# Kernel tuning notes

Hardware: AMD Instinct MI355X
Metric: run time of the kernel (lower is better)

The kernel has to match this reference:

```python
import jax, jax.numpy as jnp
import numpy as np

B, N, H, T = 4096, 512, 1024, 10  # batch, input_size, hidden_size, num_iterations
NUM_OPS = 20


def setup_inputs() -> dict:
    key = jax.random.key(0)
    k1, k2, k3, k4 = jax.random.split(key, 4)
    return {
        "x": jax.random.normal(k1, (B, N, 1), jnp.float32),
        "frozen_weight": jax.random.normal(k2, (1, N, H), jnp.float32) / np.sqrt(H),
        "alpha": jax.random.normal(k3, (T, NUM_OPS), jnp.float32),
        "layer_beta": jax.random.normal(k4, (T, 2), jnp.float32),
    }


def _softshrink(x, lam):
    return jnp.where(x > lam, x - lam, jnp.where(x < -lam, x + lam, jnp.zeros_like(x)))


def _hardshrink(x, lam):
    return jnp.where(jnp.abs(x) > lam, x, jnp.zeros_like(x))


def _make_ops(lam):
    # Same 20 ops, same order as the torch ModuleList.
    return [
        lambda x: _softshrink(x, lam),                 # Softshrink(0.001/L)
        jax.nn.relu,                                   # ReLU
        lambda x: x,                                   # Identity
        lambda x: jax.nn.gelu(x, approximate=False),   # GELU (exact erf, torch default)
        jax.nn.elu,                                    # ELU
        lambda x: _hardshrink(x, lam),                 # Hardshrink(0.001/L)
        lambda x: jnp.clip(x, -1.0, 1.0),              # Hardtanh
        jax.nn.hard_swish,                             # Hardswish
        jax.nn.selu,                                   # SELU
        jax.nn.celu,                                   # CELU
        jax.nn.leaky_relu,                             # LeakyReLU (slope 0.01)
        jax.nn.log_sigmoid,                            # LogSigmoid
        lambda x: x - jnp.tanh(x),                     # Tanhshrink
        jax.nn.soft_sign,                              # Softsign
        jax.nn.softplus,                               # Softplus
        jnp.tanh,                                      # Tanh
        jax.nn.sigmoid,                                # Sigmoid
        jax.nn.hard_sigmoid,                           # Hardsigmoid
        jax.nn.silu,                                   # SiLU
        lambda x: x * jnp.tanh(jax.nn.softplus(x)),    # Mish
    ]


def _forward(x, frozen_weight, alpha, layer_beta):
    W = frozen_weight[0]                       # [N, H]
    L = jnp.linalg.norm(W, ord=2) ** 2         # spectral norm squared (Lipschitz)
    lam = 0.001 / L
    ops = _make_ops(lam)

    b = x.shape[0]
    hidden = W.shape[1]
    z = jnp.zeros((b, hidden, 1), dtype=x.dtype)
    z_prev = z
    num_iters = alpha.shape[0]
    for i in range(num_iters):
        aw = jax.nn.softmax(alpha[i])          # [20] (training path, eval_flag=False)
        bw = jax.nn.softmax(layer_beta[i])     # [2]
        # FISTA-style momentum + frozen-weight gradient step
        z_aux = z + (i / (i + 3)) * (z - z_prev)      # [B,H,1]
        Wz = jnp.einsum('nh,bho->bno', W, z_aux)      # [B,N,1]
        grad = jnp.einsum('nh,bno->bho', W, Wz - x)   # [B,H,1]
        z_g = z_aux - grad / L
        # 20-way weighted activation mixture
        z_op = aw[0] * ops[0](z_g)
        for w, op in zip(aw[1:], ops[1:]):
            z_op = z_op + w * op(z_g)
        # beta-weighted residual mix becomes z_prev; z_op becomes current_z
        z_prev = z * bw[0] + z_op * bw[1]
        z = z_op
    return z


def reference(x, frozen_weight, alpha, layer_beta):
    return _forward(x, frozen_weight, alpha, layer_beta)
```

## Files before the change

### kernel.cpp

```cpp
#include <hip/hip_runtime.h>
#include <hip/hip_bf16.h>

#define DI __device__ __forceinline__

typedef float f32x4 __attribute__((ext_vector_type(4)));
typedef __bf16 bf16x8 __attribute__((ext_vector_type(8)));
using bf16_t = __hip_bfloat16;
using ushort_t = unsigned short;

DI void gload_lds16(const void* g, void* l) {
  __builtin_amdgcn_global_load_lds(
      (const __attribute__((address_space(1))) void*)g,
      (__attribute__((address_space(3))) void*)l, 16, 0, 0);
}

DI float rcpf(float x) { return __builtin_amdgcn_rcpf(x); }

DI float us2f(ushort_t u) {
  bf16_t h;
  *reinterpret_cast<ushort_t*>(&h) = u;
  return __bfloat162float(h);
}

DI float act_mix(float x, const float* aw, float lam) {
  const float ax  = fabsf(x);
  const float en  = __expf(-ax);
  const float en2 = en * en;
  const float i1  = rcpf(1.0f + en);
  const float sig = (x >= 0.0f) ? i1 : en * i1;
  const float th  = copysignf((1.0f - en2) * rcpf(1.0f + en2), x);
  const float l1p = __logf(1.0f + en);
  const float sp  = fmaxf(x, 0.0f) + l1p;
  const float lsg = fminf(x, 0.0f) - l1p;
  const float q   = ((x >= 0.0f) ? en2 : 1.0f) * (i1 * i1);
  const float mish = x * (1.0f - q) * rcpf(1.0f + q);
  const float u  = 0.7071067811865476f * x;
  const float au = fabsf(u);
  const float t  = rcpf(1.0f + 0.3275911f * au);
  float poly = fmaf(t, 1.061405429f, -1.453152027f);
  poly = fmaf(t, poly, 1.421413741f);
  poly = fmaf(t, poly, -0.284496736f);
  poly = fmaf(t, poly, 0.254829592f);
  poly *= t;
  const float erfa = 1.0f - poly * __expf(-u * u);
  const float gelu = 0.5f * x * (1.0f + copysignf(erfa, x));
  const float em1  = en - 1.0f;
  const float elu  = (x > 0.0f) ? x : em1;
  const float selu = (x > 0.0f) ? 1.0507009873554805f * x : 1.7580993408473766f * em1;
  const float relu = fmaxf(x, 0.0f);
  const float t6   = fminf(fmaxf(x + 3.0f, 0.0f), 6.0f) * 0.16666666666666666f;
  const float ssh  = (x > lam) ? (x - lam) : ((x < -lam) ? (x + lam) : 0.0f);
  const float hsh  = (ax > lam) ? x : 0.0f;
  const float htan = fminf(fmaxf(x, -1.0f), 1.0f);
  const float lky  = (x >= 0.0f) ? x : 0.01f * x;
  const float ssn  = x * rcpf(1.0f + ax);
  float r = aw[0] * ssh;
  r = fmaf(aw[1],  relu,   r);
  r = fmaf(aw[2],  x,      r);
  r = fmaf(aw[3],  gelu,   r);
  r = fmaf(aw[4],  elu,    r);
  r = fmaf(aw[5],  hsh,    r);
  r = fmaf(aw[6],  htan,   r);
  r = fmaf(aw[7],  x * t6, r);
  r = fmaf(aw[8],  selu,   r);
  r = fmaf(aw[9],  elu,    r);
  r = fmaf(aw[10], lky,    r);
  r = fmaf(aw[11], lsg,    r);
  r = fmaf(aw[12], x - th, r);
  r = fmaf(aw[13], ssn,    r);
  r = fmaf(aw[14], sp,     r);
  r = fmaf(aw[15], th,     r);
  r = fmaf(aw[16], sig,    r);
  r = fmaf(aw[17], t6,     r);
  r = fmaf(aw[18], x * sig, r);
  r = fmaf(aw[19], mish,   r);
  return r;
}

__global__ void k_prep(const float* __restrict__ W, const float* __restrict__ x,
                       bf16_t* __restrict__ Whi, bf16_t* __restrict__ Wlo,
                       bf16_t* __restrict__ Wth, bf16_t* __restrict__ Wtl,
                       bf16_t* __restrict__ xb) {
  int i = blockIdx.x * 256 + threadIdx.x;
  if (i < 512 * 1024) {
    float w = W[i];
    bf16_t h = __float2bfloat16(w);
    bf16_t l = __float2bfloat16(w - __bfloat162float(h));
    Whi[i] = h; Wlo[i] = l;
    int n = i >> 10, hc = i & 1023;
    Wth[hc * 512 + n] = h; Wtl[hc * 512 + n] = l;
  }
  int j = i - 512 * 1024;
  if (j >= 0 && j < 4096 * 512) xb[j] = __float2bfloat16(x[j]);
}

template <int KDIM, bool FIRST, bool DOT>
__global__ __launch_bounds__(256) void k_sqm(
    const bf16_t* __restrict__ Xhi, const bf16_t* __restrict__ Xlo,
    bf16_t* __restrict__ Chi, bf16_t* __restrict__ Clo,
    float* __restrict__ Cf,
    const float* __restrict__ pin, float* __restrict__ pout,
    float* __restrict__ numP, float* __restrict__ denP) {
  __shared__ __align__(16) ushort_t Ah[2][32 * 64], Al[2][32 * 64],
                                    Bh[2][32 * 64], Bl[2][32 * 64];
  __shared__ float red[4], redd[4];
  const int tid = threadIdx.x, lane = tid & 63, wave = tid >> 6;
  const int wm = wave >> 1, wn = wave & 1;
  const int i0 = blockIdx.x * 32, j0 = blockIdx.y * 32;
  const int bid = blockIdx.y * gridDim.x + blockIdx.x;
  const int r16 = lane & 15, kg = lane >> 4;

  float s = 1.0f;
  if constexpr (!FIRST) {
    float v = pin[tid];
    for (int off = 32; off; off >>= 1) v += __shfl_down(v, off, 64);
    if ((tid & 63) == 0) red[tid >> 6] = v;
    __syncthreads();
    s = 1.0f / (red[0] + red[1] + red[2] + red[3]);
    __syncthreads();
  }

  const int row = tid >> 3;
  const int srcc = (((tid & 7) ^ (row & 7)) << 3);
  const long abase = (long)(i0 + row) * KDIM + srcc;
  const long bbase = (long)(j0 + row) * KDIM + srcc;
  const int ldst = tid * 8;

  auto stage = [&](int buf, int kt) {
    gload_lds16(Xhi + abase + kt, &Ah[buf][ldst]);
    gload_lds16(Xlo + abase + kt, &Al[buf][ldst]);
    gload_lds16(Xhi + bbase + kt, &Bh[buf][ldst]);
    gload_lds16(Xlo + bbase + kt, &Bl[buf][ldst]);
  };

  f32x4 acc = {};
  constexpr int NT = KDIM / 64;

  auto compute = [&](int b) {
    const int ra = wm * 16 + r16, rb = wn * 16 + r16;
#pragma unroll
    for (int kk = 0; kk < 64; kk += 32) {
      int oa = ra * 64 + ((kk + kg * 8) ^ ((ra & 7) * 8));
      int ob = rb * 64 + ((kk + kg * 8) ^ ((rb & 7) * 8));
      bf16x8 ah = *(const bf16x8*)&Ah[b][oa];
      bf16x8 al = *(const bf16x8*)&Al[b][oa];
      bf16x8 bh = *(const bf16x8*)&Bh[b][ob];
      bf16x8 bl = *(const bf16x8*)&Bl[b][ob];
      acc = __builtin_amdgcn_mfma_f32_16x16x32_bf16(ah, bh, acc, 0, 0, 0);
      acc = __builtin_amdgcn_mfma_f32_16x16x32_bf16(ah, bl, acc, 0, 0, 0);
      acc = __builtin_amdgcn_mfma_f32_16x16x32_bf16(al, bh, acc, 0, 0, 0);
    }
  };

  stage(0, 0);
  stage(1, 64);
  asm volatile("s_waitcnt vmcnt(4)" ::: "memory");
  __builtin_amdgcn_s_barrier();
  __builtin_amdgcn_sched_barrier(0);

  for (int t = 0; t < NT; ++t) {
    compute(t & 1);
    if (t == NT - 1) break;
    asm volatile("s_waitcnt lgkmcnt(0)" ::: "memory");
    __builtin_amdgcn_sched_barrier(0);
    __builtin_amdgcn_s_barrier();
    if (t + 2 < NT) {
      stage(t & 1, (t + 2) * 64);
      asm volatile("s_waitcnt vmcnt(4)" ::: "memory");
    } else {
      asm volatile("s_waitcnt vmcnt(0)" ::: "memory");
    }
    __builtin_amdgcn_s_barrier();
    __builtin_amdgcn_sched_barrier(0);
  }
  __builtin_amdgcn_sched_barrier(0);

  float fro = 0.0f, dvp = 0.0f;
#pragma unroll
  for (int r = 0; r < 4; ++r) {
    float c = acc[r] * s;
    int orow = i0 + wm * 16 + (lane >> 4) * 4 + r;
    int ocol = j0 + wn * 16 + r16;
    int idx = orow * 512 + ocol;
    if constexpr (DOT) {
      fro = fmaf(Cf[idx], c, fro);
      if (orow == ocol) dvp += c;
    } else {
      bf16_t h = __float2bfloat16(c);
      Chi[idx] = h;
      Clo[idx] = __float2bfloat16(c - __bfloat162float(h));
      if constexpr (FIRST) Cf[idx] = c;
      fro = fmaf(c, c, fro);
    }
  }
  for (int off = 32; off; off >>= 1) {
    fro += __shfl_down(fro, off, 64);
    if constexpr (DOT) dvp += __shfl_down(dvp, off, 64);
  }
  if ((tid & 63) == 0) { red[tid >> 6] = fro; if constexpr (DOT) redd[tid >> 6] = dvp; }
  __syncthreads();
  if (tid == 0) {
    if constexpr (DOT) {
      numP[bid] = red[0] + red[1] + red[2] + red[3];
      denP[bid] = redd[0] + redd[1] + redd[2] + redd[3];
    } else {
      pout[bid] = red[0] + red[1] + red[2] + red[3];
    }
  }
}

__global__ __launch_bounds__(256) void k_setup(const float* __restrict__ alpha,
                                               const float* __restrict__ beta,
                                               const float* __restrict__ numP,
                                               const float* __restrict__ denP,
                                               float* __restrict__ params) {
  __shared__ float redn[4], redd[4];
  __shared__ float Lsh;
  const int tid = threadIdx.x;
  float nv = numP[tid], dv = denP[tid];
  for (int off = 32; off; off >>= 1) {
    nv += __shfl_down(nv, off, 64);
    dv += __shfl_down(dv, off, 64);
  }
  if ((tid & 63) == 0) { redn[tid >> 6] = nv; redd[tid >> 6] = dv; }
  __syncthreads();
  if (tid == 0)
    Lsh = (redn[0] + redn[1] + redn[2] + redn[3]) /
          (redd[0] + redd[1] + redd[2] + redd[3]);
  __syncthreads();
  const int t = tid;
  if (t >= 10) return;
  float L = Lsh;
  float invL = 1.0f / L;
  float lam = 0.001f * invL;
  const float* a = alpha + t * 20;
  float mx = a[0];
  for (int k = 1; k < 20; ++k) mx = fmaxf(mx, a[k]);
  float e[20], ssum = 0.0f;
  for (int k = 0; k < 20; ++k) { e[k] = expf(a[k] - mx); ssum += e[k]; }
  float inv = 1.0f / ssum;
  float* P = params + t * 32;
  for (int k = 0; k < 20; ++k) P[k] = e[k] * inv;
  float b0 = beta[t * 2], b1 = beta[t * 2 + 1];
  float bm = fmaxf(b0, b1);
  float eb0 = expf(b0 - bm), eb1 = expf(b1 - bm);
  float bw0 = eb0 / (eb0 + eb1);
  P[20] = ((float)(t + 1) / (float)(t + 4)) * bw0;
  P[21] = invL;
  P[22] = lam;
  P[23] = L;
}

__global__ __launch_bounds__(256, 4) void k_gx(
    const bf16_t* __restrict__ xb, const bf16_t* __restrict__ Wth,
    const bf16_t* __restrict__ Wtl, const float* __restrict__ prm,
    bf16_t* __restrict__ Gm, bf16_t* __restrict__ xWs,
    bf16_t* __restrict__ zB, bf16_t* __restrict__ zaux1) {
  __shared__ __align__(16) ushort_t smem[16384];
  const int tid = threadIdx.x, lane = tid & 63, wave = tid >> 6;
  const int wm = wave >> 1, wn = wave & 1;
  const int r16 = lane & 15, kg = lane >> 4;

  if ((int)blockIdx.x >= 1024) {
    const int gb = blockIdx.x - 1024;
    const int i0 = (gb & 31) * 32, j0 = (gb >> 5) * 32;
    ushort_t* Ah = smem;
    ushort_t* Al = smem + 4096;
    ushort_t* Bh = smem + 8192;
    ushort_t* Bl = smem + 12288;
    const int row = tid >> 3;
    const int srcc = (((tid & 7) ^ (row & 7)) << 3);
    const long abase = (long)(i0 + row) * 512 + srcc;
    const long bbase = (long)(j0 + row) * 512 + srcc;
    const int ldst = tid * 8;
    auto stg = [&](int buf, int kt) {
      gload_lds16(Wth + abase + kt, &Ah[buf * 2048 + ldst]);
      gload_lds16(Wtl + abase + kt, &Al[buf * 2048 + ldst]);
      gload_lds16(Wth + bbase + kt, &Bh[buf * 2048 + ldst]);
      gload_lds16(Wtl + bbase + kt, &Bl[buf * 2048 + ldst]);
    };
    f32x4 acc = {};
    stg(0, 0);
    __syncthreads();
    for (int t = 0; t < 8; ++t) {
      if (t + 1 < 8) stg((t + 1) & 1, (t + 1) * 64);
      const int b = t & 1;
      const int ra = wm * 16 + r16, rb = wn * 16 + r16;
#pragma unroll
      for (int kk = 0; kk < 64; kk += 32) {
        int oa = b * 2048 + ra * 64 + ((kk + kg * 8) ^ ((ra & 7) * 8));
        int ob = b * 2048 + rb * 64 + ((kk + kg * 8) ^ ((rb & 7) * 8));
        bf16x8 ah = *(const bf16x8*)&Ah[oa];
        bf16x8 al = *(const bf16x8*)&Al[oa];
        bf16x8 bh = *(const bf16x8*)&Bh[ob];
        bf16x8 bl = *(const bf16x8*)&Bl[ob];
        acc = __builtin_amdgcn_mfma_f32_16x16x32_bf16(ah, bh, acc, 0, 0, 0);
        acc = __builtin_amdgcn_mfma_f32_16x16x32_bf16(ah, bl, acc, 0, 0, 0);
        acc = __builtin_amdgcn_mfma_f32_16x16x32_bf16(al, bh, acc, 0, 0, 0);
      }
      __syncthreads();
    }
#pragma unroll
    for (int r = 0; r < 4; ++r) {
      int orow = i0 + wm * 16 + (lane >> 4) * 4 + r;
      int ocol = j0 + wn * 16 + r16;
      Gm[orow * 1024 + ocol] = __float2bfloat16(acc[r]);
    }
    return;
  }

  const int bid = blockIdx.x;
  const int swz = (bid & 7) * 128 + (bid >> 3);
  const int m0 = (swz >> 4) * 64, n0 = (swz & 15) * 64;
  ushort_t* As = smem;
  ushort_t* Bs = smem + 8192;

  auto stage = [&](int buf, int kt) {
#pragma unroll
    for (int q = 0; q < 2; ++q) {
      int lin = (tid + q * 256) * 8;
      int row = lin >> 6;
      int col = ((((lin >> 3) & 7) ^ (row & 7)) << 3);
      gload_lds16(xb + (long)(m0 + row) * 512 + kt + col, &As[buf * 4096 + lin]);
      gload_lds16(Wth + (long)(n0 + row) * 512 + kt + col, &Bs[buf * 4096 + lin]);
    }
  };

  f32x4 acc[2][2] = {};
  auto compute = [&](int b) {
#pragma unroll
    for (int kk = 0; kk < 64; kk += 32) {
      bf16x8 a[2], bb[2];
#pragma unroll
      for (int f = 0; f < 2; ++f) {
        int ra = wm * 32 + f * 16 + r16;
        int rb = wn * 32 + f * 16 + r16;
        a[f]  = *(const bf16x8*)&As[b * 4096 + ra * 64 + ((kk + kg * 8) ^ ((ra & 7) * 8))];
        bb[f] = *(const bf16x8*)&Bs[b * 4096 + rb * 64 + ((kk + kg * 8) ^ ((rb & 7) * 8))];
      }
#pragma unroll
      for (int i = 0; i < 2; ++i)
#pragma unroll
        for (int j = 0; j < 2; ++j)
          acc[i][j] = __builtin_amdgcn_mfma_f32_16x16x32_bf16(a[i], bb[j], acc[i][j], 0, 0, 0);
    }
  };

  stage(0, 0);
  stage(1, 64);
  asm volatile("s_waitcnt vmcnt(4)" ::: "memory");
  __builtin_amdgcn_s_barrier();
  __builtin_amdgcn_sched_barrier(0);

  for (int t = 0; t < 8; ++t) {
    compute(t & 1);
    if (t == 7) break;
    asm volatile("s_waitcnt lgkmcnt(0)" ::: "memory");
    __builtin_amdgcn_sched_barrier(0);
    __builtin_amdgcn_s_barrier();
    if (t + 2 < 8) {
      stage(t & 1, (t + 2) * 64);
      asm volatile("s_waitcnt vmcnt(4)" ::: "memory");
    } else {
      asm volatile("s_waitcnt vmcnt(0)" ::: "memory");
    }
    __builtin_amdgcn_s_barrier();
    __builtin_amdgcn_sched_barrier(0);
  }
  __builtin_amdgcn_sched_barrier(0);

  const float invL = prm[21];
  const float d0 = prm[20];
  const float lam = prm[22];
  float aw[20];
#pragma unroll
  for (int k = 0; k < 20; ++k) aw[k] = prm[k];
#pragma unroll
  for (int i = 0; i < 2; ++i)
#pragma unroll
    for (int j = 0; j < 2; ++j)
#pragma unroll
      for (int r = 0; r < 4; ++r) {
        int row = m0 + wm * 32 + i * 16 + (lane >> 4) * 4 + r;
        int col = n0 + wn * 32 + j * 16 + r16;
        long idx = (long)row * 1024 + col;
        bf16_t xv = __float2bfloat16(acc[i][j][r] * invL);
        xWs[idx] = xv;
        float zop = act_mix(__bfloat162float(xv), aw, lam);
        zB[idx] = __float2bfloat16(zop);
        zaux1[idx] = __float2bfloat16(zop * (1.0f + d0));
      }
}

template <bool LAST>
__global__ __launch_bounds__(256, 4) void k_iter(const bf16_t* __restrict__ A,
                                                 const bf16_t* __restrict__ G,
                                                 const bf16_t* __restrict__ xWs,
                                                 bf16_t* __restrict__ zauxN,
                                                 bf16_t* zB, float* zio,
                                                 const float* __restrict__ prm) {
  __shared__ __align__(16) ushort_t As[2][64 * 64], Bs[2][64 * 64];
  const int tid = threadIdx.x, lane = tid & 63, wave = tid >> 6;
  const int wm = wave >> 1, wn = wave & 1;
  const int bid = blockIdx.x;
  const int swz = (bid & 7) * 128 + (bid >> 3);
  const int m0 = (swz >> 4) * 64, n0 = (swz & 15) * 64;
  const int r16 = lane & 15, kg = lane >> 4;

  auto stage = [&](int buf, int kt) {
#pragma unroll
    for (int q = 0; q < 2; ++q) {
      int lin = (tid + q * 256) * 8;
      int row = lin >> 6;
      int col = ((((lin >> 3) & 7) ^ (row & 7)) << 3);
      gload_lds16(A + (long)(m0 + row) * 1024 + kt + col, &As[buf][lin]);
      gload_lds16(G + (long)(n0 + row) * 1024 + kt + col, &Bs[buf][lin]);
    }
  };

  f32x4 acc[2][2] = {};
  auto compute = [&](int b) {
#pragma unroll
    for (int kk = 0; kk < 64; kk += 32) {
      bf16x8 a[2], bb[2];
#pragma unroll
      for (int f = 0; f < 2; ++f) {
        int ra = wm * 32 + f * 16 + r16;
        int rb = wn * 32 + f * 16 + r16;
        a[f]  = *(const bf16x8*)&As[b][ra * 64 + ((kk + kg * 8) ^ ((ra & 7) * 8))];
        bb[f] = *(const bf16x8*)&Bs[b][rb * 64 + ((kk + kg * 8) ^ ((rb & 7) * 8))];
      }
#pragma unroll
      for (int i = 0; i < 2; ++i)
#pragma unroll
        for (int j = 0; j < 2; ++j)
          acc[i][j] = __builtin_amdgcn_mfma_f32_16x16x32_bf16(a[i], bb[j], acc[i][j], 0, 0, 0);
    }
  };

  const int snap_t = n0 >> 6;
  ushort_t ar[2][2][4];

  stage(0, 0);
  stage(1, 64);
  asm volatile("s_waitcnt vmcnt(4)" ::: "memory");
  __builtin_amdgcn_s_barrier();
  __builtin_amdgcn_sched_barrier(0);

  for (int t = 0; t < 16; ++t) {
    compute(t & 1);
    if (t == snap_t) {
#pragma unroll
      for (int i = 0; i < 2; ++i)
#pragma unroll
        for (int j = 0; j < 2; ++j)
#pragma unroll
          for (int r = 0; r < 4; ++r) {
            int rl = wm * 32 + i * 16 + (lane >> 4) * 4 + r;
            int cl = wn * 32 + j * 16 + r16;
            ar[i][j][r] = As[t & 1][rl * 64 + (cl ^ ((rl & 7) * 8))];
          }
    }
    if (t == 15) break;
    asm volatile("s_waitcnt lgkmcnt(0)" ::: "memory");
    __builtin_amdgcn_sched_barrier(0);
    __builtin_amdgcn_s_barrier();
    if (t + 2 < 16) {
      stage(t & 1, (t + 2) * 64);
      asm volatile("s_waitcnt vmcnt(4)" ::: "memory");
    } else {
      asm volatile("s_waitcnt vmcnt(0)" ::: "memory");
    }
    __builtin_amdgcn_s_barrier();
    __builtin_amdgcn_sched_barrier(0);
  }
  __builtin_amdgcn_sched_barrier(0);

  const float d_i = prm[20];
  const float invL = prm[21];
  const float lam = prm[22];
  float aw[20];
#pragma unroll
  for (int k = 0; k < 20; ++k) aw[k] = prm[k];

  float xv[2][2][4], zv[2][2][4];
#pragma unroll
  for (int i = 0; i < 2; ++i)
#pragma unroll
    for (int j = 0; j < 2; ++j)
#pragma unroll
      for (int r = 0; r < 4; ++r) {
        int row = m0 + wm * 32 + i * 16 + (lane >> 4) * 4 + r;
        int col = n0 + wn * 32 + j * 16 + r16;
        long idx = (long)row * 1024 + col;
        xv[i][j][r] = __bfloat162float(xWs[idx]);
        if (!LAST) zv[i][j][r] = __bfloat162float(zB[idx]);
      }
#pragma unroll
  for (int i = 0; i < 2; ++i)
#pragma unroll
    for (int j = 0; j < 2; ++j)
#pragma unroll
      for (int r = 0; r < 4; ++r) {
        int row = m0 + wm * 32 + i * 16 + (lane >> 4) * 4 + r;
        int col = n0 + wn * 32 + j * 16 + r16;
        long idx = (long)row * 1024 + col;
        float zg = fmaf(-acc[i][j][r], invL, us2f(ar[i][j][r]) + xv[i][j][r]);
        float zop = act_mix(zg, aw, lam);
        if (LAST) {
          zio[idx] = zop;
        } else {
          zB[idx] = __float2bfloat16(zop);
          zauxN[idx] = __float2bfloat16(fmaf(d_i, zop - zv[i][j][r], zop));
        }
      }
}

extern "C" void kernel_launch(void* const* d_in, const int* in_sizes, int n_in,
                              void* d_out, int out_size, void* d_ws, size_t ws_size,
                              hipStream_t stream) {
  const float* x     = (const float*)d_in[0];
  const float* W     = (const float*)d_in[1];
  const float* alpha = (const float*)d_in[2];
  const float* beta  = (const float*)d_in[3];
  float* zout = (float*)d_out;

  char* ws = (char*)d_ws;
  const size_t MB = 1u << 20;
  float* pb[9];
  for (int k = 0; k < 9; ++k) pb[k] = (float*)(ws + (size_t)k * 1024);
  float* numP   = (float*)(ws + 10 * 1024);
  float* denP   = (float*)(ws + 11 * 1024);
  float* params = (float*)(ws + 12 * 1024);
  const size_t HDR = 32768;
  float*  A0f  = (float*)(ws + HDR);
  bf16_t* H0   = (bf16_t*)(ws + HDR + 2 * MB);
  bf16_t* L0   = (bf16_t*)(ws + HDR + 2 * MB + 512 * 1024);
  bf16_t* H1   = (bf16_t*)(ws + HDR + 3 * MB);
  bf16_t* L1   = (bf16_t*)(ws + HDR + 3 * MB + 512 * 1024);
  bf16_t* Whi  = (bf16_t*)(ws + HDR + 4 * MB);
  bf16_t* Wlo  = (bf16_t*)(ws + HDR + 5 * MB);
  bf16_t* Wth  = (bf16_t*)(ws + HDR + 6 * MB);
  bf16_t* Wtl  = (bf16_t*)(ws + HDR + 7 * MB);
  bf16_t* Gm   = (bf16_t*)(ws + HDR + 8 * MB);
  bf16_t* xb   = (bf16_t*)(ws + HDR + 10 * MB);
  bf16_t* xWs  = (bf16_t*)(ws + HDR + 18 * MB);
  bf16_t* zx0  = (bf16_t*)(ws + HDR + 26 * MB);
  bf16_t* zx1  = (bf16_t*)(ws + HDR + 34 * MB);
  bf16_t* zB   = (bf16_t*)(ws + HDR + 42 * MB);

  k_prep<<<10240, 256, 0, stream>>>(W, x, Whi, Wlo, Wth, Wtl, xb);

  k_sqm<1024, true, false><<<dim3(16, 16), 256, 0, stream>>>(
      Whi, Wlo, H0, L0, A0f, nullptr, pb[0], nullptr, nullptr);
  bf16_t* Hs[2] = {H0, H1};
  bf16_t* Ls[2] = {L0, L1};
  int pp = 0;
  for (int k = 0; k < 7; ++k) {
    k_sqm<512, false, false><<<dim3(16, 16), 256, 0, stream>>>(
        Hs[pp], Ls[pp], Hs[pp ^ 1], Ls[pp ^ 1], nullptr, pb[k], pb[k + 1],
        nullptr, nullptr);
    pp ^= 1;
  }
  k_sqm<512, false, true><<<dim3(16, 16), 256, 0, stream>>>(
      Hs[pp], Ls[pp], nullptr, nullptr, A0f, pb[7], nullptr, numP, denP);
  k_setup<<<1, 256, 0, stream>>>(alpha, beta, numP, denP, params);

  k_gx<<<2048, 256, 0, stream>>>(xb, Wth, Wtl, params, Gm, xWs, zB, zx1);

  bf16_t* zx[2] = {zx0, zx1};
  for (int i = 1; i < 9; ++i)
    k_iter<false><<<1024, 256, 0, stream>>>(zx[i & 1], Gm, xWs, zx[(i + 1) & 1],
                                            zB, zout, params + i * 32);
  k_iter<true><<<1024, 256, 0, stream>>>(zx[9 & 1], Gm, xWs, zx0 ,
                                         zB, zout, params + 9 * 32);
}
```

Before: 339.9 us.

## Fuse spectral-norm squaring chain into one persistent kernel with grid barriers

Replaces the ten separate launches (nine repeated-squaring matmul kernels plus the setup kernel) with a single persistent 256-block kernel. Dependent phases are separated by a software grid barrier built on atomic flags, and the workspace holds per-phase partial sums and barrier flags, which are zeroed with a memset. This is meant to remove per-launch overhead and launch gaps on the serial dependency chain. In exchange it relies on all 256 blocks being co-resident for the spin barrier to avoid deadlock, and adds the cost of the memset and atomic polling.

```diff
diff --git a/kernel.cpp b/kernel.cpp
--- a/kernel.cpp
+++ b/kernel.cpp
@@ -94,161 +94,192 @@
   if (j >= 0 && j < 4096 * 512) xb[j] = __float2bfloat16(x[j]);
 }
 
-template <int KDIM, bool FIRST, bool DOT>
-__global__ __launch_bounds__(256) void k_sqm(
-    const bf16_t* __restrict__ Xhi, const bf16_t* __restrict__ Xlo,
-    bf16_t* __restrict__ Chi, bf16_t* __restrict__ Clo,
-    float* __restrict__ Cf,
-    const float* __restrict__ pin, float* __restrict__ pout,
-    float* __restrict__ numP, float* __restrict__ denP) {
-  __shared__ __align__(16) ushort_t Ah[2][32 * 64], Al[2][32 * 64],
-                                    Bh[2][32 * 64], Bl[2][32 * 64];
+__global__ __launch_bounds__(256, 1) void k_Lchain(
+    const bf16_t* __restrict__ Whi, const bf16_t* __restrict__ Wlo,
+    bf16_t* __restrict__ H0, bf16_t* __restrict__ L0,
+    bf16_t* __restrict__ H1, bf16_t* __restrict__ L1,
+    float* __restrict__ A0f, float* __restrict__ pb,
+    float* __restrict__ numP, float* __restrict__ denP,
+    const float* __restrict__ alpha, const float* __restrict__ beta,
+    float* __restrict__ params, int* flags, int* gen) {
+  __shared__ __align__(16) ushort_t Ah[2][2048], Al[2][2048],
+                                    Bh[2][2048], Bl[2][2048];
   __shared__ float red[4], redd[4];
   const int tid = threadIdx.x, lane = tid & 63, wave = tid >> 6;
   const int wm = wave >> 1, wn = wave & 1;
-  const int i0 = blockIdx.x * 32, j0 = blockIdx.y * 32;
-  const int bid = blockIdx.y * gridDim.x + blockIdx.x;
+  const int bid = blockIdx.x;
+  const int i0 = (bid & 15) * 32, j0 = (bid >> 4) * 32;
   const int r16 = lane & 15, kg = lane >> 4;
-
-  float s = 1.0f;
-  if constexpr (!FIRST) {
-    float v = pin[tid];
-    for (int off = 32; off; off >>= 1) v += __shfl_down(v, off, 64);
-    if ((tid & 63) == 0) red[tid >> 6] = v;
-    __syncthreads();
-    s = 1.0f / (red[0] + red[1] + red[2] + red[3]);
-    __syncthreads();
-  }
-
   const int row = tid >> 3;
   const int srcc = (((tid & 7) ^ (row & 7)) << 3);
-  const long abase = (long)(i0 + row) * KDIM + srcc;
-  const long bbase = (long)(j0 + row) * KDIM + srcc;
   const int ldst = tid * 8;
 
-  auto stage = [&](int buf, int kt) {
-    gload_lds16(Xhi + abase + kt, &Ah[buf][ldst]);
-    gload_lds16(Xlo + abase + kt, &Al[buf][ldst]);
-    gload_lds16(Xhi + bbase + kt, &Bh[buf][ldst]);
-    gload_lds16(Xlo + bbase + kt, &Bl[buf][ldst]);
+  auto gbar = [&](int g) {
+    __syncthreads();
+    __threadfence();
+    if (tid == 0)
+      __hip_atomic_store(&flags[bid], g, __ATOMIC_RELEASE, __HIP_MEMORY_SCOPE_AGENT);
+    if (bid == 0) {
+      while (__hip_atomic_load(&flags[tid], __ATOMIC_ACQUIRE,
+                               __HIP_MEMORY_SCOPE_AGENT) < g) {}
+      __syncthreads();
+      if (tid == 0)
+        __hip_atomic_store(gen, g, __ATOMIC_RELEASE, __HIP_MEMORY_SCOPE_AGENT);
+    } else {
+      if (tid == 0)
+        while (__hip_atomic_load(gen, __ATOMIC_ACQUIRE,
+                                 __HIP_MEMORY_SCOPE_AGENT) < g) {}
+      __syncthreads();
+    }
+    __threadfence();
   };
 
-  f32x4 acc = {};
-  constexpr int NT = KDIM / 64;
-
-  auto compute = [&](int b) {
-    const int ra = wm * 16 + r16, rb = wn * 16 + r16;
-#pragma unroll
-    for (int kk = 0; kk < 64; kk += 32) {
-      int oa = ra * 64 + ((kk + kg * 8) ^ ((ra & 7) * 8));
-      int ob = rb * 64 + ((kk + kg * 8) ^ ((rb & 7) * 8));
-      bf16x8 ah = *(const bf16x8*)&Ah[b][oa];
-      bf16x8 al = *(const bf16x8*)&Al[b][oa];
-      bf16x8 bh = *(const bf16x8*)&Bh[b][ob];
-      bf16x8 bl = *(const bf16x8*)&Bl[b][ob];
-      acc = __builtin_amdgcn_mfma_f32_16x16x32_bf16(ah, bh, acc, 0, 0, 0);
-      acc = __builtin_amdgcn_mfma_f32_16x16x32_bf16(ah, bl, acc, 0, 0, 0);
-      acc = __builtin_amdgcn_mfma_f32_16x16x32_bf16(al, bh, acc, 0, 0, 0);
-    }
-  };
-
-  stage(0, 0);
-  stage(1, 64);
-  asm volatile("s_waitcnt vmcnt(4)" ::: "memory");
-  __builtin_amdgcn_s_barrier();
-  __builtin_amdgcn_sched_barrier(0);
-
-  for (int t = 0; t < NT; ++t) {
-    compute(t & 1);
-    if (t == NT - 1) break;
-    asm volatile("s_waitcnt lgkmcnt(0)" ::: "memory");
-    __builtin_amdgcn_sched_barrier(0);
-    __builtin_amdgcn_s_barrier();
-    if (t + 2 < NT) {
-      stage(t & 1, (t + 2) * 64);
-      asm volatile("s_waitcnt vmcnt(4)" ::: "memory");
-    } else {
-      asm volatile("s_waitcnt vmcnt(0)" ::: "memory");
-    }
+  auto phase = [&](const bf16_t* Xhi, const bf16_t* Xlo, int KDIM,
+                   bf16_t* Chi, bf16_t* Clo, bool first, bool dot,
+                   const float* pin, float* pout) {
+    float s = 1.0f;
+    if (!first) {
+      float v = pin[tid];
+      for (int off = 32; off; off >>= 1) v += __shfl_down(v, off, 64);
+      if ((tid & 63) == 0) red[tid >> 6] = v;
+      __syncthreads();
+      s = 1.0f / (red[0] + red[1] + red[2] + red[3]);
+      __syncthreads();
+    }
+    const long abase = (long)(i0 + row) * KDIM + srcc;
+    const long bbase = (long)(j0 + row) * KDIM + srcc;
+    auto stage = [&](int buf, int kt) {
+      gload_lds16(Xhi + abase + kt, &Ah[buf][ldst]);
+      gload_lds16(Xlo + abase + kt, &Al[buf][ldst]);
+      gload_lds16(Xhi + bbase + kt, &Bh[buf][ldst]);
+      gload_lds16(Xlo + bbase + kt, &Bl[buf][ldst]);
+    };
+    f32x4 acc = {};
+    const int NT = KDIM / 64;
+    auto compute = [&](int b) {
+      const int ra = wm * 16 + r16, rb = wn * 16 + r16;
+#pragma unroll
+      for (int kk = 0; kk < 64; kk += 32) {
+        int oa = ra * 64 + ((kk + kg * 8) ^ ((ra & 7) * 8));
+        int ob = rb * 64 + ((kk + kg * 8) ^ ((rb & 7) * 8));
+        bf16x8 ah = *(const bf16x8*)&Ah[b][oa];
+        bf16x8 al = *(const bf16x8*)&Al[b][oa];
+        bf16x8 bh = *(const bf16x8*)&Bh[b][ob];
+        bf16x8 bl = *(const bf16x8*)&Bl[b][ob];
+        acc = __builtin_amdgcn_mfma_f32_16x16x32_bf16(ah, bh, acc, 0, 0, 0);
+        acc = __builtin_amdgcn_mfma_f32_16x16x32_bf16(ah, bl, acc, 0, 0, 0);
+        acc = __builtin_amdgcn_mfma_f32_16x16x32_bf16(al, bh, acc, 0, 0, 0);
+      }
+    };
+
+    stage(0, 0);
+    stage(1, 64);
+    asm volatile("s_waitcnt vmcnt(4)" ::: "memory");
     __builtin_amdgcn_s_barrier();
     __builtin_amdgcn_sched_barrier(0);
+    for (int t = 0; t < NT; ++t) {
+      compute(t & 1);
+      if (t == NT - 1) break;
+      asm volatile("s_waitcnt lgkmcnt(0)" ::: "memory");
+      __builtin_amdgcn_sched_barrier(0);
+      __builtin_amdgcn_s_barrier();
+      if (t + 2 < NT) {
+        stage(t & 1, (t + 2) * 64);
+        asm volatile("s_waitcnt vmcnt(4)" ::: "memory");
+      } else {
+        asm volatile("s_waitcnt vmcnt(0)" ::: "memory");
+      }
+      __builtin_amdgcn_s_barrier();
+      __builtin_amdgcn_sched_barrier(0);
+    }
+    __builtin_amdgcn_sched_barrier(0);
+
+    float fro = 0.0f, dvp = 0.0f;
+#pragma unroll
+    for (int r = 0; r < 4; ++r) {
+      float c = acc[r] * s;
+      int orow = i0 + wm * 16 + (lane >> 4) * 4 + r;
+      int ocol = j0 + wn * 16 + r16;
+      int idx = orow * 512 + ocol;
+      if (dot) {
+        fro = fmaf(A0f[idx], c, fro);
+        if (orow == ocol) dvp += c;
+      } else {
+        bf16_t h = __float2bfloat16(c);
+        Chi[idx] = h;
+        Clo[idx] = __float2bfloat16(c - __bfloat162float(h));
+        if (first) A0f[idx] = c;
+        fro = fmaf(c, c, fro);
+      }
+    }
+    for (int off = 32; off; off >>= 1) {
+      fro += __shfl_down(fro, off, 64);
+      if (dot) dvp += __shfl_down(dvp, off, 64);
+    }
+    if ((tid & 63) == 0) { red[tid >> 6] = fro; if (dot) redd[tid >> 6] = dvp; }
+    __syncthreads();
+    if (tid == 0) {
+      if (dot) {
+        numP[bid] = red[0] + red[1] + red[2] + red[3];
+        denP[bid] = redd[0] + redd[1] + redd[2] + redd[3];
+      } else {
+        pout[bid] = red[0] + red[1] + red[2] + red[3];
+      }
+    }
+  };
+
+  phase(Whi, Wlo, 1024, H0, L0, true, false, nullptr, pb);
+  gbar(1);
+  bf16_t* Hs[2] = {H0, H1};
+  bf16_t* Ls[2] = {L0, L1};
+  int pp = 0;
+  for (int k = 0; k < 7; ++k) {
+    phase(Hs[pp], Ls[pp], 512, Hs[pp ^ 1], Ls[pp ^ 1], false, false,
+          pb + k * 256, pb + (k + 1) * 256);
+    gbar(k + 2);
+    pp ^= 1;
   }
-  __builtin_amdgcn_sched_barrier(0);
-
-  float fro = 0.0f, dvp = 0.0f;
-#pragma unroll
-  for (int r = 0; r < 4; ++r) {
-    float c = acc[r] * s;
-    int orow = i0 + wm * 16 + (lane >> 4) * 4 + r;
-    int ocol = j0 + wn * 16 + r16;
-    int idx = orow * 512 + ocol;
-    if constexpr (DOT) {
-      fro = fmaf(Cf[idx], c, fro);
-      if (orow == ocol) dvp += c;
-    } else {
-      bf16_t h = __float2bfloat16(c);
-      Chi[idx] = h;
-      Clo[idx] = __float2bfloat16(c - __bfloat162float(h));
-      if constexpr (FIRST) Cf[idx] = c;
-      fro = fmaf(c, c, fro);
-    }
+  phase(Hs[pp], Ls[pp], 512, nullptr, nullptr, false, true,
+        pb + 7 * 256, nullptr);
+  gbar(9);
+
+  if (bid != 0) return;
+  {
+    __shared__ float redn2[4], redd2[4];
+    __shared__ float Lsh;
+    float nv = numP[tid], dv = denP[tid];
+    for (int off = 32; off; off >>= 1) {
+      nv += __shfl_down(nv, off, 64);
+      dv += __shfl_down(dv, off, 64);
+    }
+    if ((tid & 63) == 0) { redn2[tid >> 6] = nv; redd2[tid >> 6] = dv; }
+    __syncthreads();
+    if (tid == 0)
+      Lsh = (redn2[0] + redn2[1] + redn2[2] + redn2[3]) /
+            (redd2[0] + redd2[1] + redd2[2] + redd2[3]);
+    __syncthreads();
+    const int t = tid;
+    if (t >= 10) return;
+    float L = Lsh;
+    float invL = 1.0f / L;
+    float lam = 0.001f * invL;
+    const float* a = alpha + t * 20;
+    float mx = a[0];
+    for (int k = 1; k < 20; ++k) mx = fmaxf(mx, a[k]);
+    float e[20], ssum = 0.0f;
+    for (int k = 0; k < 20; ++k) { e[k] = expf(a[k] - mx); ssum += e[k]; }
+    float inv = 1.0f / ssum;
+    float* P = params + t * 32;
+    for (int k = 0; k < 20; ++k) P[k] = e[k] * inv;
+    float b0 = beta[t * 2], b1 = beta[t * 2 + 1];
+    float bm = fmaxf(b0, b1);
+    float eb0 = expf(b0 - bm), eb1 = expf(b1 - bm);
+    float bw0 = eb0 / (eb0 + eb1);
+    P[20] = ((float)(t + 1) / (float)(t + 4)) * bw0;
+    P[21] = invL;
+    P[22] = lam;
+    P[23] = L;
   }
-  for (int off = 32; off; off >>= 1) {
-    fro += __shfl_down(fro, off, 64);
-    if constexpr (DOT) dvp += __shfl_down(dvp, off, 64);
-  }
-  if ((tid & 63) == 0) { red[tid >> 6] = fro; if constexpr (DOT) redd[tid >> 6] = dvp; }
-  __syncthreads();
-  if (tid == 0) {
-    if constexpr (DOT) {
-      numP[bid] = red[0] + red[1] + red[2] + red[3];
-      denP[bid] = redd[0] + redd[1] + redd[2] + redd[3];
-    } else {
-      pout[bid] = red[0] + red[1] + red[2] + red[3];
-    }
-  }
-}
-
-__global__ __launch_bounds__(256) void k_setup(const float* __restrict__ alpha,
-                                               const float* __restrict__ beta,
-                                               const float* __restrict__ numP,
-                                               const float* __restrict__ denP,
-                                               float* __restrict__ params) {
-  __shared__ float redn[4], redd[4];
-  __shared__ float Lsh;
-  const int tid = threadIdx.x;
-  float nv = numP[tid], dv = denP[tid];
-  for (int off = 32; off; off >>= 1) {
-    nv += __shfl_down(nv, off, 64);
-    dv += __shfl_down(dv, off, 64);
-  }
-  if ((tid & 63) == 0) { redn[tid >> 6] = nv; redd[tid >> 6] = dv; }
-  __syncthreads();
-  if (tid == 0)
-    Lsh = (redn[0] + redn[1] + redn[2] + redn[3]) /
-          (redd[0] + redd[1] + redd[2] + redd[3]);
-  __syncthreads();
-  const int t = tid;
-  if (t >= 10) return;
-  float L = Lsh;
-  float invL = 1.0f / L;
-  float lam = 0.001f * invL;
-  const float* a = alpha + t * 20;
-  float mx = a[0];
-  for (int k = 1; k < 20; ++k) mx = fmaxf(mx, a[k]);
-  float e[20], ssum = 0.0f;
-  for (int k = 0; k < 20; ++k) { e[k] = expf(a[k] - mx); ssum += e[k]; }
-  float inv = 1.0f / ssum;
-  float* P = params + t * 32;
-  for (int k = 0; k < 20; ++k) P[k] = e[k] * inv;
-  float b0 = beta[t * 2], b1 = beta[t * 2 + 1];
-  float bm = fmaxf(b0, b1);
-  float eb0 = expf(b0 - bm), eb1 = expf(b1 - bm);
-  float bw0 = eb0 / (eb0 + eb1);
-  P[20] = ((float)(t + 1) / (float)(t + 4)) * bw0;
-  P[21] = invL;
-  P[22] = lam;
-  P[23] = L;
 }
 
 __global__ __launch_bounds__(256, 4) void k_gx(
@@ -527,11 +558,12 @@
 
   char* ws = (char*)d_ws;
   const size_t MB = 1u << 20;
-  float* pb[9];
-  for (int k = 0; k < 9; ++k) pb[k] = (float*)(ws + (size_t)k * 1024);
+  float* pb     = (float*)(ws);
   float* numP   = (float*)(ws + 10 * 1024);
   float* denP   = (float*)(ws + 11 * 1024);
   float* params = (float*)(ws + 12 * 1024);
+  int*   flags  = (int*)(ws + 14 * 1024);
+  int*   gen    = (int*)(ws + 15 * 1024);
   const size_t HDR = 32768;
   float*  A0f  = (float*)(ws + HDR);
   bf16_t* H0   = (bf16_t*)(ws + HDR + 2 * MB);
@@ -549,22 +581,13 @@
   bf16_t* zx1  = (bf16_t*)(ws + HDR + 34 * MB);
   bf16_t* zB   = (bf16_t*)(ws + HDR + 42 * MB);
 
+  hipMemsetAsync(ws + 14 * 1024, 0, 2048, stream);
+
   k_prep<<<10240, 256, 0, stream>>>(W, x, Whi, Wlo, Wth, Wtl, xb);
 
-  k_sqm<1024, true, false><<<dim3(16, 16), 256, 0, stream>>>(
-      Whi, Wlo, H0, L0, A0f, nullptr, pb[0], nullptr, nullptr);
-  bf16_t* Hs[2] = {H0, H1};
-  bf16_t* Ls[2] = {L0, L1};
-  int pp = 0;
-  for (int k = 0; k < 7; ++k) {
-    k_sqm<512, false, false><<<dim3(16, 16), 256, 0, stream>>>(
-        Hs[pp], Ls[pp], Hs[pp ^ 1], Ls[pp ^ 1], nullptr, pb[k], pb[k + 1],
-        nullptr, nullptr);
-    pp ^= 1;
-  }
-  k_sqm<512, false, true><<<dim3(16, 16), 256, 0, stream>>>(
-      Hs[pp], Ls[pp], nullptr, nullptr, A0f, pb[7], nullptr, numP, denP);
-  k_setup<<<1, 256, 0, stream>>>(alpha, beta, numP, denP, params);
+  k_Lchain<<<256, 256, 0, stream>>>(Whi, Wlo, H0, L0, H1, L1, A0f, pb,
+                                    numP, denP, alpha, beta, params,
+                                    flags, gen);
 
   k_gx<<<2048, 256, 0, stream>>>(xb, Wth, Wtl, params, Gm, xWs, zB, zx1);
 
```

Result: slower. 875.1 us (+157.4%).
